# Optimization experiments

Measured on AMD Instinct MI355X. Metric: run time of the kernel, lower is better.

## Reference

```python
import jax, jax.numpy as jnp
import numpy as np

NUM_CLASSES = 21
IOU_THR = 0.5
SCORE_THR = 0.04


def _conv(x, w, b, stride):
    # NCHW / OIHW, SAME padding
    y = jax.lax.conv_general_dilated(
        x, w, (stride, stride), 'SAME',
        dimension_numbers=('NCHW', 'OIHW', 'NCHW'))
    return y + b[None, :, None, None]


def _pairwise_iou(boxes):
    # original module which feeds locs straight into ops.nms.
    x1, y1, x2, y2 = boxes[:, 0], boxes[:, 1], boxes[:, 2], boxes[:, 3]
    area = (x2 - x1) * (y2 - y1)
    lt_x = jnp.maximum(x1[:, None], x1[None, :])
    lt_y = jnp.maximum(y1[:, None], y1[None, :])
    rb_x = jnp.minimum(x2[:, None], x2[None, :])
    rb_y = jnp.minimum(y2[:, None], y2[None, :])
    inter = jnp.clip(rb_x - lt_x, 0.0) * jnp.clip(rb_y - lt_y, 0.0)
    union = area[:, None] + area[None, :] - inter
    return inter / (union + 1e-9)


def _nms_keep(boxes, scores, valid):
    # Greedy NMS over score-sorted candidates; padded/masked, jit-friendly.
    order = jnp.argsort(-scores)
    b = boxes[order]            # [N,4]
    v = valid[order]            # [N]
    iou = _pairwise_iou(b)      # [N,N]
    n = boxes.shape[0]

    def body(i, keep):
        suppressed = jnp.any(keep & (iou[i] > IOU_THR))
        return keep.at[i].set(v[i] & jnp.logical_not(suppressed))

    keep = jax.lax.fori_loop(0, n, body, jnp.zeros((n,), bool))
    return order, keep


def _ssd_forward(x, bb_w1, bb_b1, bb_w2, bb_b2, bb_w3, bb_b3,
                 ex_w, ex_b, reg_w, reg_b, cls_w, cls_b):
    # backbone: three stride-2 conv+relu blocks
    h = jax.nn.relu(_conv(x, bb_w1, bb_b1, 2))
    h = jax.nn.relu(_conv(h, bb_w2, bb_b2, 2))
    h = jax.nn.relu(_conv(h, bb_w3, bb_b3, 2))
    # extras: one stride-2 conv+relu
    h = jax.nn.relu(_conv(h, ex_w, ex_b, 2))
    # heads
    locs = _conv(h, reg_w, reg_b, 1)    # [B, 4, H, W]
    confs = _conv(h, cls_w, cls_b, 1)   # [B, C, H, W]
    B = locs.shape[0]
    locs = jnp.transpose(locs, (0, 2, 3, 1)).reshape(B, -1, 4)        # [B, N, 4]
    confs = jnp.transpose(confs, (0, 2, 3, 1)).reshape(B, -1, NUM_CLASSES)  # [B, N, C]

    # PostProcessor: softmax -> max -> threshold mask -> NMS, vectorized over batch
    probs = jax.nn.softmax(confs, axis=-1)
    scores = jnp.max(probs, axis=-1)      # [B, N]
    labels = jnp.argmax(probs, axis=-1)   # [B, N]
    valid = scores > SCORE_THR

    order, keep = jax.vmap(_nms_keep)(locs, scores, valid)  # [B,N], [B,N] bool

    # The original's buggy inner loop leaves only the LAST image's results.
    i = B - 1
    o, k = order[i], keep[i]
    b_s = locs[i][o]
    s_s = scores[i][o]
    l_s = labels[i][o]
    c_s = confs[i][o]
    out_boxes = jnp.where(k[:, None], b_s, -1.0)
    out_labels = jnp.where(k, l_s, 0).astype(jnp.int64)
    out_scores = jnp.where(k, s_s, -1.0)
    out_confs = jnp.where(k[:, None], c_s, -1.0)
    return out_boxes, out_labels, out_scores, out_confs


def setup_inputs() -> dict:
    key = jax.random.key(0)
    ks = jax.random.split(key, 8)

    def w(k, shape):
        fan_in = shape[1] * shape[2] * shape[3]
        return jax.random.normal(k, shape, jnp.float32) / np.sqrt(fan_in)

    x = jax.random.normal(ks[0], (8, 3, 512, 512), jnp.float32)
    return {
        'x': x,
        'bb_w1': w(ks[1], (64, 3, 3, 3)),   'bb_b1': jnp.zeros((64,), jnp.float32),
        'bb_w2': w(ks[2], (128, 64, 3, 3)), 'bb_b2': jnp.zeros((128,), jnp.float32),
        'bb_w3': w(ks[3], (256, 128, 3, 3)),'bb_b3': jnp.zeros((256,), jnp.float32),
        'ex_w':  w(ks[4], (256, 256, 3, 3)),'ex_b':  jnp.zeros((256,), jnp.float32),
        'reg_w': w(ks[5], (4, 256, 3, 3)),  'reg_b': jnp.zeros((4,), jnp.float32),
        'cls_w': w(ks[6], (NUM_CLASSES, 256, 3, 3)), 'cls_b': jnp.zeros((NUM_CLASSES,), jnp.float32),
    }


def reference(x, bb_w1, bb_b1, bb_w2, bb_b2, bb_w3, bb_b3,
              ex_w, ex_b, reg_w, reg_b, cls_w, cls_b):
    return _ssd_forward(x, bb_w1, bb_b1, bb_w2, bb_b2, bb_w3, bb_b3,
                        ex_w, ex_b, reg_w, reg_b, cls_w, cls_b)
```

## Files before the change

kernel.cpp:

```cpp
#include <hip/hip_runtime.h>
#include <cstdint>
#include <cstddef>


__global__ __launch_bounds__(256) void k_repack_all(
    const float* __restrict__ w2, const float* __restrict__ w3,
    const float* __restrict__ w4, const float* __restrict__ regw,
    const float* __restrict__ clsw, float* __restrict__ wr2,
    float* __restrict__ wr3, float* __restrict__ wr4, float* __restrict__ wh) {
  int idx = blockIdx.x * 256 + threadIdx.x;
  if (idx < 73728) {
    int co = idx % 128, r = idx / 128, ci = r / 9, tap = r % 9;
    wr2[idx] = w2[(co * 64 + ci) * 9 + tap];
  } else if (idx < 73728 + 294912) {
    int i = idx - 73728;
    int co = i % 256, r = i / 256, ci = r / 9, tap = r % 9;
    wr3[i] = w3[(co * 128 + ci) * 9 + tap];
  } else if (idx < 73728 + 294912 + 589824) {
    int i = idx - (73728 + 294912);
    int co = i % 256, r = i / 256, ci = r / 9, tap = r % 9;
    wr4[i] = w4[(co * 256 + ci) * 9 + tap];
  } else if (idx < 73728 + 294912 + 589824 + 57600) {
    int i = idx - (73728 + 294912 + 589824);
    int ci = i & 255, r = i >> 8, tap = r / 25, o = r % 25;
    wh[i] = (o < 4) ? regw[(o * 256 + ci) * 9 + tap]
                    : clsw[((o - 4) * 256 + ci) * 9 + tap];
  }
}

__global__ __launch_bounds__(256) void k_conv1(const float* __restrict__ x,
                                               const float* __restrict__ w,
                                               const float* __restrict__ b,
                                               float* __restrict__ out) {
  __shared__ float in_t[3][33][33];
  const int tx = threadIdx.x, ty = threadIdx.y;
  const int tid = ty * 16 + tx;
  const int ox0 = blockIdx.x * 16, oy0 = blockIdx.y * 16;
  const int co0 = blockIdx.z * 8;
  for (int idx = tid; idx < 3 * 33 * 33; idx += 256) {
    int ci = idx / 1089, rem = idx % 1089;
    int r = rem / 33, c = rem % 33;
    int iy = oy0 * 2 + r, ix = ox0 * 2 + c;
    float v = 0.f;
    if (iy < 512 && ix < 512) v = x[(size_t)ci * 262144 + iy * 512 + ix];
    in_t[ci][r][c] = v;
  }
  __syncthreads();
  float rin[27];
#pragma unroll
  for (int ci = 0; ci < 3; ++ci)
#pragma unroll
    for (int kh = 0; kh < 3; ++kh)
#pragma unroll
      for (int kw = 0; kw < 3; ++kw)
        rin[ci * 9 + kh * 3 + kw] = in_t[ci][2 * ty + kh][2 * tx + kw];
  const int oy = oy0 + ty, ox = ox0 + tx;
  for (int co = co0; co < co0 + 8; ++co) {
    float a = 0.f;
#pragma unroll
    for (int k = 0; k < 27; ++k) a = fmaf(w[co * 27 + k], rin[k], a);
    out[(size_t)co * 65536 + oy * 256 + ox] = fmaxf(a + b[co], 0.f);
  }
}

template <int CIN, int COUT, int HIN, int WIN, int SH, int SW, int COPT,
          int CIT, int KSPLIT, int ROWW, int NW>
__global__ __launch_bounds__(NW * 64, 4) void conv_s2(
    const float* __restrict__ in, const float* __restrict__ wr,
    const float* __restrict__ bias, float* __restrict__ out) {
  constexpr int HOUT = HIN / 2, WOUT = WIN / 2;
  constexpr int IH = SH * 2 + 1, IW = SW * 2 + 1;
  constexpr int EVW = SW + 1;
  constexpr int COT = NW * COPT;
  constexpr int NPAIR = CIT * IH * EVW;
  constexpr int NTHR = NW * 64;
  constexpr int NLD = (NPAIR + NTHR - 1) / NTHR;
  static_assert(SH * SW == 64, "one position per lane");
  static_assert(EVW + SW < ROWW + 1, "pad slot fits");
  __shared__ float lds[CIT * IH * ROWW];

  const int tid = threadIdx.x;
  const int gu  = __builtin_amdgcn_readfirstlane(tid >> 6);
  const int lp  = tid & 63;
  const int py  = lp / SW, px = lp % SW;

  constexpr int ntx = WOUT / SW;
  const int bx = blockIdx.x % ntx, by = blockIdx.x / ntx;
  const int ox0 = bx * SW, oy0 = by * SH;
  const int co_blk = blockIdx.y * COT;
  const int cobase = co_blk + gu * COPT;
  const int ci_begin = (KSPLIT > 1) ? blockIdx.z * (CIN / KSPLIT) : 0;
  constexpr int NST = (CIN / KSPLIT) / CIT;

  unsigned goff[NLD];
  int      loff[NLD];
  int      mode[NLD];
#pragma unroll
  for (int j = 0; j < NLD; ++j) {
    int idx = tid + j * NTHR;
    bool act = (idx < NPAIR);
    int ci = idx / (IH * EVW), rem = idx % (IH * EVW);
    int r = rem / EVW, c2 = rem % EVW;
    int iy = oy0 * 2 + r, ix = ox0 * 2 + 2 * c2;
    loff[j] = act ? (ci * IH + r) * ROWW + c2 : -1;
    goff[j] = (unsigned)((ci_begin + ci) * HIN * WIN + iy * WIN + ix);
    int m = 0;
    if (act && iy < HIN) {
      if ((2 * c2 + 1 < IW) && (ix + 1 < WIN)) m = 1;
      else if (ix < WIN) m = 2;
    }
    mode[j] = m;
  }

  float2 pre[NLD];
#pragma unroll
  for (int j = 0; j < NLD; ++j) {
    float2 t = make_float2(0.f, 0.f);
    if (mode[j] == 1)      t = *(const float2*)(in + goff[j]);
    else if (mode[j] == 2) t.x = in[goff[j]];
    pre[j] = t;
  }

  float acc[COPT] = {};

  unsigned adv = (unsigned)(CIT * HIN * WIN);
  for (int st = 0; st < NST; ++st, adv += (unsigned)(CIT * HIN * WIN)) {
    const int cib = ci_begin + st * CIT;
    if (st) __syncthreads();
#pragma unroll
    for (int j = 0; j < NLD; ++j) {
      if (loff[j] >= 0) {
        lds[loff[j]] = pre[j].x;
        lds[loff[j] + EVW] = pre[j].y;
      }
    }
    if (st + 1 < NST) {
#pragma unroll
      for (int j = 0; j < NLD; ++j) {
        float2 t = make_float2(0.f, 0.f);
        if (mode[j] == 1)      t = *(const float2*)(in + goff[j] + adv);
        else if (mode[j] == 2) t.x = in[goff[j] + adv];
        pre[j] = t;
      }
    }
    __syncthreads();
#pragma unroll 2
    for (int ci = 0; ci < CIT; ++ci) {
      const int b0 = (ci * IH + 2 * py) * ROWW + px;
      float e00 = lds[b0];
      float q0  = lds[b0 + EVW];
      float e01 = lds[b0 + 1];
      float e10 = lds[b0 + ROWW];
      float q1  = lds[b0 + ROWW + EVW];
      float e11 = lds[b0 + ROWW + 1];
      float e20 = lds[b0 + 2 * ROWW];
      float q2  = lds[b0 + 2 * ROWW + EVW];
      float e21 = lds[b0 + 2 * ROWW + 1];
      const float* wp = wr + (size_t)(cib + ci) * 9 * COUT + cobase;
#pragma unroll
      for (int c = 0; c < COPT; ++c) acc[c] = fmaf(e00, wp[c], acc[c]);
#pragma unroll
      for (int c = 0; c < COPT; ++c) acc[c] = fmaf(q0, wp[COUT + c], acc[c]);
#pragma unroll
      for (int c = 0; c < COPT; ++c) acc[c] = fmaf(e01, wp[2 * COUT + c], acc[c]);
#pragma unroll
      for (int c = 0; c < COPT; ++c) acc[c] = fmaf(e10, wp[3 * COUT + c], acc[c]);
#pragma unroll
      for (int c = 0; c < COPT; ++c) acc[c] = fmaf(q1, wp[4 * COUT + c], acc[c]);
#pragma unroll
      for (int c = 0; c < COPT; ++c) acc[c] = fmaf(e11, wp[5 * COUT + c], acc[c]);
#pragma unroll
      for (int c = 0; c < COPT; ++c) acc[c] = fmaf(e20, wp[6 * COUT + c], acc[c]);
#pragma unroll
      for (int c = 0; c < COPT; ++c) acc[c] = fmaf(q2, wp[7 * COUT + c], acc[c]);
#pragma unroll
      for (int c = 0; c < COPT; ++c) acc[c] = fmaf(e21, wp[8 * COUT + c], acc[c]);
    }
  }

  const int oy = oy0 + py, ox = ox0 + px;
#pragma unroll
  for (int c = 0; c < COPT; ++c) {
    int co = cobase + c;
    if constexpr (KSPLIT > 1) {
      out[((size_t)blockIdx.z * COUT + co) * (HOUT * WOUT) + oy * WOUT + ox] =
          acc[c];
    } else {
      out[(size_t)co * (HOUT * WOUT) + oy * WOUT + ox] =
          fmaxf(acc[c] + bias[co], 0.f);
    }
  }
}

__global__ __launch_bounds__(256) void k_combine(const float* __restrict__ part,
                                                 const float* __restrict__ b,
                                                 float* __restrict__ h4t) {
  int co = blockIdx.x;
  float bb = b[co];
  for (int k2 = 0; k2 < 4; ++k2) {
    int pos = threadIdx.x + k2 * 256;
    float v = part[(size_t)(0 * 256 + co) * 1024 + pos] +
              part[(size_t)(1 * 256 + co) * 1024 + pos] +
              part[(size_t)(2 * 256 + co) * 1024 + pos] +
              part[(size_t)(3 * 256 + co) * 1024 + pos];
    h4t[(size_t)pos * 256 + co] = fmaxf(v + bb, 0.f);
  }
}

__global__ __launch_bounds__(256) void k_head(const float* __restrict__ h4t,
                                              const float* __restrict__ wh,
                                              const float* __restrict__ regb,
                                              const float* __restrict__ clsb,
                                              float* __restrict__ locs,
                                              float* __restrict__ confs,
                                              float* __restrict__ scores,
                                              float* __restrict__ labelsF) {
  const int pos = blockIdx.x;
  const int py = pos >> 5, px = pos & 31;
  const int t = threadIdx.x;
  float part[25] = {};
#pragma unroll
  for (int kh = 0; kh < 3; ++kh) {
    int iy = py + kh - 1;
    if (iy < 0 || iy > 31) continue;
#pragma unroll
    for (int kw = 0; kw < 3; ++kw) {
      int ix = px + kw - 1;
      if (ix < 0 || ix > 31) continue;
      int tap = kh * 3 + kw;
      float v = h4t[(size_t)(iy * 32 + ix) * 256 + t];
      const float* wp = wh + (size_t)tap * 25 * 256 + t;
#pragma unroll
      for (int o = 0; o < 25; ++o)
        part[o] = fmaf(v, wp[(size_t)o * 256], part[o]);
    }
  }
#pragma unroll
  for (int o = 0; o < 25; ++o) {
#pragma unroll
    for (int d = 1; d < 64; d <<= 1) part[o] += __shfl_xor(part[o], d);
  }
  __shared__ float red[4][25];
  __shared__ float yv[25];
  const int wv = t >> 6, ln = t & 63;
  if (ln == 0) {
#pragma unroll
    for (int o = 0; o < 25; ++o) red[wv][o] = part[o];
  }
  __syncthreads();
  if (t < 25) {
    float y = red[0][t] + red[1][t] + red[2][t] + red[3][t];
    y += (t < 4) ? regb[t] : clsb[t - 4];
    if (t < 4) locs[(size_t)pos * 4 + t] = y;
    else       confs[(size_t)pos * 21 + (t - 4)] = y;
    yv[t] = y;
  }
  __syncthreads();
  if (t == 0) {
    float m = yv[4];
    int lab = 0;
    for (int j = 1; j < 21; ++j)
      if (yv[4 + j] > m) { m = yv[4 + j]; lab = j; }
    float s = 0.f;
    for (int j = 0; j < 21; ++j) s += expf(yv[4 + j] - m);
    scores[pos] = 1.f / s;
    labelsF[pos] = (float)lab;
  }
}

__global__ __launch_bounds__(512) void k_sort(const float* __restrict__ scores,
                                              const float* __restrict__ locs,
                                              int* __restrict__ order,
                                              float* __restrict__ ssc,
                                              float* __restrict__ bsrt,
                                              unsigned long long* __restrict__ vbits) {
  __shared__ float sk[1024];
  __shared__ int   si[1024];
  const int t = threadIdx.x;
  sk[t] = scores[t];           si[t] = t;
  sk[t + 512] = scores[t + 512]; si[t + 512] = t + 512;
  for (int k = 2; k <= 1024; k <<= 1) {
    for (int j = k >> 1; j > 0; j >>= 1) {
      __syncthreads();
      int i1 = ((t / j) * (2 * j)) + (t % j);
      int i2 = i1 + j;
      bool up = (i1 & k) == 0;
      float sa = sk[i1], sb = sk[i2];
      int ia = si[i1], ib = si[i2];
      bool b_before_a = (sb > sa) || (sb == sa && ib < ia);
      bool a_before_b = (sa > sb) || (sa == sb && ia < ib);
      bool sw = up ? b_before_a : a_before_b;
      if (sw) { sk[i1] = sb; sk[i2] = sa; si[i1] = ib; si[i2] = ia; }
    }
  }
  __syncthreads();
  for (int i = t; i < 1024; i += 512) {
    int oi = si[i];
    order[i] = oi;
    ssc[i] = sk[i];
    ((float4*)bsrt)[i] = ((const float4*)locs)[oi];
  }
  if (t < 16) {
    unsigned long long w = 0;
    for (int b2 = 0; b2 < 64; ++b2)
      if (sk[t * 64 + b2] > 0.04f) w |= (1ull << b2);
    vbits[t] = w;
  }
}

__global__ __launch_bounds__(256) void k_mask(const float* __restrict__ bsrt,
                                              unsigned long long* __restrict__ mask) {
  __shared__ float4 sb[1024];
  const int t = threadIdx.x;
  for (int idx = t; idx < 1024; idx += 256)
    sb[idx] = ((const float4*)bsrt)[idx];
  __syncthreads();
  const int i = blockIdx.x * 16 + (t & 15);
  const int w = t >> 4;
  float4 bi = sb[i];
  float ai = (bi.z - bi.x) * (bi.w - bi.y);
  unsigned long long bits = 0;
  for (int jj = 0; jj < 64; ++jj) {
    float4 bj = sb[w * 64 + jj];
    float aj = (bj.z - bj.x) * (bj.w - bj.y);
    float ltx = fmaxf(bi.x, bj.x), lty = fmaxf(bi.y, bj.y);
    float rbx = fminf(bi.z, bj.z), rby = fminf(bi.w, bj.w);
    float inter = fmaxf(rbx - ltx, 0.f) * fmaxf(rby - lty, 0.f);
    float uni = ai + aj - inter;
    float iou = inter / (uni + 1e-9f);
    if (iou > 0.5f) bits |= (1ull << jj);
  }
  mask[(size_t)i * 16 + w] = bits;
}

__global__ __launch_bounds__(1024) void k_nms_gather(
    const unsigned long long* __restrict__ mask,
    const unsigned long long* __restrict__ vbits,
    const int* __restrict__ order, const float* __restrict__ ssc,
    const float* __restrict__ locs, const float* __restrict__ confs,
    const float* __restrict__ labelsF, float* __restrict__ out) {
  __shared__ unsigned long long KEEP[16], DEAD[16];
  __shared__ int ncert;
  const int i = threadIdx.x;
  const int w = i >> 6, l = i & 63;

  unsigned long long R[16];
#pragma unroll
  for (int k = 0; k < 16; ++k) {
    unsigned long long m = 0;
    if (k < w) m = mask[(size_t)i * 16 + k];
    else if (k == w && l) m = mask[(size_t)i * 16 + k] & ((1ull << l) - 1ull);
    R[k] = m;
  }
  const bool valid = (vbits[w] >> l) & 1ull;

  if (i < 16) { KEEP[i] = 0ull; DEAD[i] = 0ull; }
  if (i == 0) ncert = 0;
  __syncthreads();

  int status = 0;
  for (;;) {
    unsigned long long s = 0, p = 0;
    if (status == 0) {
#pragma unroll
      for (int k = 0; k < 16; ++k) {
        unsigned long long K_ = KEEP[k], D_ = DEAD[k];
        s |= R[k] & K_;
        p |= R[k] & ~D_;
      }
    }
    __syncthreads();
    bool newKeep = false, newDead = false;
    if (status == 0) {
      if (!valid)      { status = 2; newDead = true; }
      else if (s)      { status = 2; newDead = true; }
      else if (!p)     { status = 1; newKeep = true; }
    }
    unsigned long long bk = __ballot(newKeep);
    unsigned long long bd = __ballot(newDead);
    if (l == 0) {
      if (bk) KEEP[w] |= bk;
      if (bd) DEAD[w] |= bd;
      int n = __popcll(bk) + __popcll(bd);
      if (n) atomicAdd(&ncert, n);
    }
    __syncthreads();
    if (ncert >= 1024) break;
  }

  const bool kp = (status == 1);
  const int oi = order[i];
  float4 bx = kp ? ((const float4*)locs)[oi]
                 : make_float4(-1.f, -1.f, -1.f, -1.f);
  ((float4*)out)[i] = bx;
  out[4096 + i] = kp ? labelsF[oi] : 0.f;
  out[5120 + i] = kp ? ssc[i] : -1.f;
  float* oc = out + 6144 + (size_t)i * 21;
  const float* cc = confs + (size_t)oi * 21;
#pragma unroll
  for (int c = 0; c < 21; ++c) oc[c] = kp ? cc[c] : -1.f;
}

extern "C" void kernel_launch(void* const* d_in, const int* in_sizes, int n_in,
                              void* d_out, int out_size, void* d_ws, size_t ws_size,
                              hipStream_t stream) {
  const float* x    = (const float*)d_in[0] + (size_t)7 * 3 * 512 * 512;
  const float* w1   = (const float*)d_in[1];
  const float* b1   = (const float*)d_in[2];
  const float* w2   = (const float*)d_in[3];
  const float* b2   = (const float*)d_in[4];
  const float* w3   = (const float*)d_in[5];
  const float* b3   = (const float*)d_in[6];
  const float* w4   = (const float*)d_in[7];
  const float* b4   = (const float*)d_in[8];
  const float* regw = (const float*)d_in[9];
  const float* regb = (const float*)d_in[10];
  const float* clsw = (const float*)d_in[11];
  const float* clsb = (const float*)d_in[12];
  float* out = (float*)d_out;
  char* ws = (char*)d_ws;

  float* h1    = (float*)(ws + 0);
  float* part4 = (float*)(ws + 0);
  float* h4t   = (float*)(ws + 9437184);
  float* h2    = (float*)(ws + 16777216);
  float* h3    = (float*)(ws + 25165824);
  float* wr2   = (float*)(ws + 29360128);
  float* wr3   = (float*)(ws + 29655040);
  float* wr4   = (float*)(ws + 30834688);
  float* wh    = (float*)(ws + 33193984);
  float* locs  = (float*)(ws + 33424384);
  float* confs = (float*)(ws + 33440768);
  float* scores  = (float*)(ws + 33526784);
  float* labelsF = (float*)(ws + 33530880);
  int*   order   = (int*)  (ws + 33534976);
  float* ssc     = (float*)(ws + 33539072);
  float* bsrt    = (float*)(ws + 33543168);
  unsigned long long* mask  = (unsigned long long*)(ws + 33559552);
  unsigned long long* vbits = (unsigned long long*)(ws + 33690624);

  k_repack_all<<<3969, 256, 0, stream>>>(w2, w3, w4, regw, clsw,
                                         wr2, wr3, wr4, wh);

  k_conv1<<<dim3(16, 16, 8), dim3(16, 16), 0, stream>>>(x, w1, b1, h1);

  conv_s2<64, 128, 256, 256, 4, 16, 8, 16, 1, 36, 4>
      <<<dim3(256, 4, 1), 256, 0, stream>>>(h1, wr2, b2, h2);
  conv_s2<128, 256, 128, 128, 8, 8, 4, 16, 1, 20, 4>
      <<<dim3(64, 16, 1), 256, 0, stream>>>(h2, wr3, b3, h3);
  conv_s2<256, 256, 64, 64, 8, 8, 4, 16, 4, 20, 4>
      <<<dim3(16, 16, 4), 256, 0, stream>>>(h3, wr4, (const float*)nullptr, part4);
  k_combine<<<256, 256, 0, stream>>>(part4, b4, h4t);

  k_head<<<1024, 256, 0, stream>>>(h4t, wh, regb, clsb, locs, confs, scores, labelsF);

  k_sort<<<1, 512, 0, stream>>>(scores, locs, order, ssc, bsrt, vbits);
  k_mask<<<64, 256, 0, stream>>>(bsrt, mask);
  k_nms_gather<<<1, 1024, 0, stream>>>(mask, vbits, order, ssc, locs, confs,
                                       labelsF, out);
}
```

Before: 369.1 us.

## Stage conv weight tiles in LDS with register prefetch instead of global reads

The stride-2 conv kernel now loads each CIT-channel slice of repacked weights cooperatively into shared memory as float4 chunks. The next slice is prefetched into registers alongside the input tile, and the inner loop reads weights from LDS with broadcast float4 loads instead of scalar global loads. This removes the repeated per-wave global/scalar-cache weight traffic in the FMA loop. In exchange it uses more LDS and more registers for the prefetch, which may lower occupancy.

```diff
diff --git a/kernel.cpp b/kernel.cpp
--- a/kernel.cpp
+++ b/kernel.cpp
@@ -75,9 +75,15 @@
   constexpr int NPAIR = CIT * IH * EVW;
   constexpr int NTHR = NW * 64;
   constexpr int NLD = (NPAIR + NTHR - 1) / NTHR;
+  constexpr int NC4 = COPT / 4;
+  constexpr int CO4 = COT / 4;
+  constexpr int W4  = CIT * 9 * CO4;
+  constexpr int NLW = (W4 + NTHR - 1) / NTHR;
   static_assert(SH * SW == 64, "one position per lane");
   static_assert(EVW + SW < ROWW + 1, "pad slot fits");
+  static_assert(COPT % 4 == 0, "float4 weight chunks");
   __shared__ float lds[CIT * IH * ROWW];
+  __shared__ float4 wlds4[W4];
 
   const int tid = threadIdx.x;
   const int gu  = __builtin_amdgcn_readfirstlane(tid >> 6);
@@ -112,6 +118,16 @@
     mode[j] = m;
   }
 
+  unsigned wgoff[NLW];
+  bool     wok[NLW];
+#pragma unroll
+  for (int j = 0; j < NLW; ++j) {
+    int widx = tid + j * NTHR;
+    wok[j] = (widx < W4);
+    int row = widx / CO4, cw4 = widx % CO4;
+    wgoff[j] = (unsigned)((ci_begin * 9 + row) * COUT + co_blk + cw4 * 4);
+  }
+
   float2 pre[NLD];
 #pragma unroll
   for (int j = 0; j < NLD; ++j) {
@@ -120,12 +136,17 @@
     else if (mode[j] == 2) t.x = in[goff[j]];
     pre[j] = t;
   }
+  float4 wpre[NLW];
+#pragma unroll
+  for (int j = 0; j < NLW; ++j)
+    if (wok[j]) wpre[j] = *(const float4*)(wr + wgoff[j]);
 
   float acc[COPT] = {};
 
-  unsigned adv = (unsigned)(CIT * HIN * WIN);
-  for (int st = 0; st < NST; ++st, adv += (unsigned)(CIT * HIN * WIN)) {
-    const int cib = ci_begin + st * CIT;
+  constexpr unsigned IADV = (unsigned)(CIT * HIN * WIN);
+  constexpr unsigned WADV = (unsigned)(CIT * 9 * COUT);
+  unsigned iadv = IADV, wadv = WADV;
+  for (int st = 0; st < NST; ++st, iadv += IADV, wadv += WADV) {
     if (st) __syncthreads();
 #pragma unroll
     for (int j = 0; j < NLD; ++j) {
@@ -134,47 +155,47 @@
         lds[loff[j] + EVW] = pre[j].y;
       }
     }
+#pragma unroll
+    for (int j = 0; j < NLW; ++j)
+      if (wok[j]) wlds4[tid + j * NTHR] = wpre[j];
+    __syncthreads();
     if (st + 1 < NST) {
 #pragma unroll
       for (int j = 0; j < NLD; ++j) {
         float2 t = make_float2(0.f, 0.f);
-        if (mode[j] == 1)      t = *(const float2*)(in + goff[j] + adv);
-        else if (mode[j] == 2) t.x = in[goff[j] + adv];
+        if (mode[j] == 1)      t = *(const float2*)(in + goff[j] + iadv);
+        else if (mode[j] == 2) t.x = in[goff[j] + iadv];
         pre[j] = t;
       }
-    }
-    __syncthreads();
+#pragma unroll
+      for (int j = 0; j < NLW; ++j)
+        if (wok[j]) wpre[j] = *(const float4*)(wr + wgoff[j] + wadv);
+    }
 #pragma unroll 2
     for (int ci = 0; ci < CIT; ++ci) {
       const int b0 = (ci * IH + 2 * py) * ROWW + px;
-      float e00 = lds[b0];
-      float q0  = lds[b0 + EVW];
-      float e01 = lds[b0 + 1];
-      float e10 = lds[b0 + ROWW];
-      float q1  = lds[b0 + ROWW + EVW];
-      float e11 = lds[b0 + ROWW + 1];
-      float e20 = lds[b0 + 2 * ROWW];
-      float q2  = lds[b0 + 2 * ROWW + EVW];
-      float e21 = lds[b0 + 2 * ROWW + 1];
-      const float* wp = wr + (size_t)(cib + ci) * 9 * COUT + cobase;
-#pragma unroll
-      for (int c = 0; c < COPT; ++c) acc[c] = fmaf(e00, wp[c], acc[c]);
-#pragma unroll
-      for (int c = 0; c < COPT; ++c) acc[c] = fmaf(q0, wp[COUT + c], acc[c]);
-#pragma unroll
-      for (int c = 0; c < COPT; ++c) acc[c] = fmaf(e01, wp[2 * COUT + c], acc[c]);
-#pragma unroll
-      for (int c = 0; c < COPT; ++c) acc[c] = fmaf(e10, wp[3 * COUT + c], acc[c]);
-#pragma unroll
-      for (int c = 0; c < COPT; ++c) acc[c] = fmaf(q1, wp[4 * COUT + c], acc[c]);
-#pragma unroll
-      for (int c = 0; c < COPT; ++c) acc[c] = fmaf(e11, wp[5 * COUT + c], acc[c]);
-#pragma unroll
-      for (int c = 0; c < COPT; ++c) acc[c] = fmaf(e20, wp[6 * COUT + c], acc[c]);
-#pragma unroll
-      for (int c = 0; c < COPT; ++c) acc[c] = fmaf(q2, wp[7 * COUT + c], acc[c]);
-#pragma unroll
-      for (int c = 0; c < COPT; ++c) acc[c] = fmaf(e21, wp[8 * COUT + c], acc[c]);
+      float in9[9];
+      in9[0] = lds[b0];
+      in9[1] = lds[b0 + EVW];
+      in9[2] = lds[b0 + 1];
+      in9[3] = lds[b0 + ROWW];
+      in9[4] = lds[b0 + ROWW + EVW];
+      in9[5] = lds[b0 + ROWW + 1];
+      in9[6] = lds[b0 + 2 * ROWW];
+      in9[7] = lds[b0 + 2 * ROWW + EVW];
+      in9[8] = lds[b0 + 2 * ROWW + 1];
+      const int wb = ci * 9 * CO4 + gu * NC4;
+#pragma unroll
+      for (int t = 0; t < 9; ++t) {
+#pragma unroll
+        for (int q = 0; q < NC4; ++q) {
+          float4 wv = wlds4[wb + t * CO4 + q];
+          acc[q * 4 + 0] = fmaf(in9[t], wv.x, acc[q * 4 + 0]);
+          acc[q * 4 + 1] = fmaf(in9[t], wv.y, acc[q * 4 + 1]);
+          acc[q * 4 + 2] = fmaf(in9[t], wv.z, acc[q * 4 + 2]);
+          acc[q * 4 + 3] = fmaf(in9[t], wv.w, acc[q * 4 + 3]);
+        }
+      }
     }
   }
 
```

New measurement: 408.3 us. 10.6% more time.
